# Performance work log

Measured on AMD Instinct MI355X. Metric: run time of the kernel, lower is better.

## Reference

```python
import math
import jax, jax.numpy as jnp
import numpy as np

B, N, NR, DA, E, H, NB = 2, 2048, 256, 256, 768, 12, 2
DH = E // H
NQ, NK = 32, 128
INF = 1e10


def _layernorm(x, g=None, b=None, eps=1e-5):
    mu = x.mean(-1, keepdims=True)
    var = ((x - mu) ** 2).mean(-1, keepdims=True)
    y = (x - mu) * jax.lax.rsqrt(var + eps)
    if g is not None:
        y = y * g + b
    return y


def _fourier(x):
    # NeRF-style: freqs = 2**linspace(0,12,64); out dim = 3*(1+2*64) = 387
    freqs = 2.0 ** jnp.linspace(0.0, 12.0, 64)
    ang = (x[..., None, :] * freqs[:, None]).reshape(*x.shape[:-1], -1)  # (...,192)
    return jnp.concatenate([x, jnp.sin(ang), jnp.cos(ang)], -1)


def _abs_pos(pos):
    # sinusoidal absolute PE, embed_dim=DA//2, include_input -> DA//2 + 1 dims
    d = DA // 2
    div = jnp.exp(jnp.arange(0, d, 2, dtype=jnp.float32) * (-math.log(10000.0) / d))
    ang = pos * div  # (B,N,1)*(d/2,) -> (B,N,d/2)
    return jnp.concatenate([pos, jnp.sin(ang), jnp.cos(ang)], -1)


def _local_bias(n, nq, nk):
    # vectorized create_local_attn_bias: block-diagonal local window mask
    i = jnp.arange(n)
    blk = i // nq
    lo = jnp.maximum(0, nq * blk - (nk - nq) // 2)
    hi = nq * blk + (nq + nk) // 2
    j = jnp.arange(n)
    allowed = (j[None, :] >= lo[:, None]) & (j[None, :] < hi[:, None])
    return jnp.where(allowed, 0.0, -INF).astype(jnp.float32)


def _rope(x, pos):
    # x: (B,H,N,DH), pos: (B,N) float
    half = DH // 2
    inv = 1.0 / (10000.0 ** (jnp.arange(half, dtype=jnp.float32) / half))
    ang = pos[:, None, :, None] * inv  # (B,1,N,half)
    c, s = jnp.cos(ang), jnp.sin(ang)
    x1, x2 = x[..., :half], x[..., half:]
    return jnp.concatenate([x1 * c - x2 * s, x1 * s + x2 * c], -1)


def setup_inputs() -> dict:
    key = jax.random.key(0)
    def rn(i, shape, s=1.0):
        return jax.random.normal(jax.random.fold_in(key, i), shape, jnp.float32) * s
    LF = 387 + (DA // 2 + 1) + 408  # 924
    tok = (jnp.arange(N) * NR) // N  # each atom's residue index (sorted)
    inp = {
        'atom_coords': rn(0, (B, N, 3), 10.0),
        'ref_pos': rn(1, (B, N, 3), 10.0),
        'res_id': jnp.broadcast_to(tok[None, :, None], (B, N, 1)).astype(jnp.int32),
        'res_type_feat': rn(2, (B, N, 23)),
        'charge': rn(3, (B, N, 1)),
        'atomic_number': rn(4, (B, N, 128)),
        'atom_name_feat': rn(5, (B, N, 256)),
        'adaLN_emb': rn(6, (B, DA)),
        'rope_pos': jnp.broadcast_to(jnp.arange(N, dtype=jnp.int32)[None], (B, N)),
        'atom_to_token': jnp.broadcast_to(jax.nn.one_hot(tok, NR, dtype=jnp.float32)[None], (B, N, NR)),
        'feat_W': rn(7, (LF, DA), 0.02), 'feat_b': jnp.zeros(DA), 'feat_ln_g': jnp.ones(DA), 'feat_ln_b': jnp.zeros(DA),
        'pos_W': rn(8, (387, DA), 0.02),
        'in_W': rn(9, (2 * DA, DA), 0.02),
        'tin_W': rn(10, (DA, E), 0.02), 'tin_b': jnp.zeros(E), 'tin_ln_g': jnp.ones(E), 'tin_ln_b': jnp.zeros(E),
        'ada_W': rn(11, (DA, E), 0.02), 'ada_b': jnp.zeros(E), 'ada_ln_g': jnp.ones(E), 'ada_ln_b': jnp.zeros(E),
        'blk_mod_W': rn(12, (NB, E, 6 * E), 0.02), 'blk_mod_b': jnp.zeros((NB, 6 * E)),
        'blk_qkv_W': rn(13, (NB, E, 3 * E), 0.02), 'blk_qkv_b': jnp.zeros((NB, 3 * E)),
        'blk_o_W': rn(14, (NB, E, E), 0.02), 'blk_o_b': jnp.zeros((NB, E)),
        'blk_m1_W': rn(15, (NB, E, 4 * E), 0.02), 'blk_m1_b': jnp.zeros((NB, 4 * E)),
        'blk_m2_W': rn(16, (NB, 4 * E, E), 0.02), 'blk_m2_b': jnp.zeros((NB, E)),
        'tout_W': rn(17, (E, DA), 0.02), 'tout_b': jnp.zeros(DA), 'tout_ln_g': jnp.ones(DA), 'tout_ln_b': jnp.zeros(DA),
    }
    return inp


def reference(atom_coords, ref_pos, res_id, res_type_feat, charge, atomic_number,
              atom_name_feat, adaLN_emb, rope_pos, atom_to_token,
              feat_W, feat_b, feat_ln_g, feat_ln_b, pos_W, in_W,
              tin_W, tin_b, tin_ln_g, tin_ln_b, ada_W, ada_b, ada_ln_g, ada_ln_b,
              blk_mod_W, blk_mod_b, blk_qkv_W, blk_qkv_b, blk_o_W, blk_o_b,
              blk_m1_W, blk_m1_b, blk_m2_W, blk_m2_b,
              tout_W, tout_b, tout_ln_g, tout_ln_b):
    # feature fusion
    ref_pos_emb = _fourier(ref_pos)                                   # (B,N,387)
    atom_res_pos = _abs_pos(res_id.astype(jnp.float32))               # (B,N,129)
    feats = jnp.concatenate([ref_pos_emb, res_type_feat, atom_res_pos,
                             charge, atomic_number, atom_name_feat], -1)  # (B,N,924)
    feats = jax.nn.silu(_layernorm(feats @ feat_W + feat_b, feat_ln_g, feat_ln_b))
    coords = _fourier(atom_coords) @ pos_W                            # (B,N,DA)
    atom_in = jnp.concatenate([feats, coords], -1) @ in_W             # (B,N,DA)
    x = _layernorm(atom_in @ tin_W + tin_b, tin_ln_g, tin_ln_b)       # (B,N,E)
    c = _layernorm(adaLN_emb @ ada_W + ada_b, ada_ln_g, ada_ln_b)     # (B,E)

    bias = _local_bias(N, NQ, NK)                                     # (N,N)
    pos = rope_pos.astype(jnp.float32)
    scale = 1.0 / math.sqrt(DH)
    for l in range(NB):  # small fixed layer count
        m = jax.nn.silu(c) @ blk_mod_W[l] + blk_mod_b[l]
        sh1, sc1, g1, sh2, sc2, g2 = jnp.split(m, 6, -1)              # each (B,E)
        h = _layernorm(x) * (1 + sc1[:, None]) + sh1[:, None]
        qkv = (h @ blk_qkv_W[l] + blk_qkv_b[l]).reshape(B, N, 3, H, DH)
        q, k, v = [qkv[:, :, i].transpose(0, 2, 1, 3) for i in range(3)]  # (B,H,N,DH)
        q, k = _rope(q, pos), _rope(k, pos)
        scores = jnp.einsum('bhqd,bhkd->bhqk', q, k) * scale + bias
        attn = jax.nn.softmax(scores, -1)
        o = jnp.einsum('bhqk,bhkd->bhqd', attn, v).transpose(0, 2, 1, 3).reshape(B, N, E)
        x = x + g1[:, None] * (o @ blk_o_W[l] + blk_o_b[l])
        h2 = _layernorm(x) * (1 + sc2[:, None]) + sh2[:, None]
        x = x + g2[:, None] * (jax.nn.gelu(h2 @ blk_m1_W[l] + blk_m1_b[l]) @ blk_m2_W[l] + blk_m2_b[l])

    atom_latent = _layernorm(x @ tout_W + tout_b, tout_ln_g, tout_ln_b)   # (B,N,DA)
    a2t = atom_to_token / (atom_to_token.sum(1, keepdims=True) + 1e-6)    # segment-mean weights
    residue_latent = jnp.einsum('bnr,bnd->brd', a2t, atom_latent)         # (B,NR,DA)
    return residue_latent, atom_latent
```

## Files before the change

### kernel.cpp

```cpp
#include <hip/hip_runtime.h>
#include <hip/hip_bf16.h>
#include <math.h>

#define B_ 2
#define N_ 2048
#define NR_ 256
#define DA_ 256
#define E_ 768
#define H_ 12
#define DH_ 64
#define NB_ 2

typedef __attribute__((ext_vector_type(8))) __bf16 bf16x8;
typedef __attribute__((ext_vector_type(4))) float f32x4;

union U8 { bf16x8 v; __hip_bfloat16 e[8]; unsigned short u[8]; };
union U4 { __hip_bfloat16 e[4]; uint2 u2; };

__device__ __forceinline__ void gload16(const void* g, void* l) {
    __builtin_amdgcn_global_load_lds(
        (const __attribute__((address_space(1))) void*)g,
        (__attribute__((address_space(3))) void*)l, 16, 0, 0);
}

__device__ __forceinline__ float bsum256(float v, float* red4, int tid) {
    #pragma unroll
    for (int m = 32; m > 0; m >>= 1) v += __shfl_xor(v, m, 64);
    __syncthreads();
    if ((tid & 63) == 0) red4[tid >> 6] = v;
    __syncthreads();
    return red4[0] + red4[1] + red4[2] + red4[3];
}

__global__ __launch_bounds__(128) void build_feats_kernel(
    const float* __restrict__ atom_coords, const float* __restrict__ ref_pos,
    const int* __restrict__ res_id, const float* __restrict__ res_type,
    const float* __restrict__ charge, const float* __restrict__ atomic_number,
    const float* __restrict__ atom_name, const int* __restrict__ rope_pos,
    __hip_bfloat16* __restrict__ feats, __hip_bfloat16* __restrict__ coordsF,
    float* __restrict__ ropeC, float* __restrict__ ropeS)
{
    int a = blockIdx.x;
    int tid = threadIdx.x;
    __hip_bfloat16* f  = feats   + (size_t)a * 1024;
    __hip_bfloat16* cf = coordsF + (size_t)a * 512;

    float rp[3], cc[3];
    #pragma unroll
    for (int i = 0; i < 3; ++i) { rp[i] = ref_pos[(size_t)a*3 + i]; cc[i] = atom_coords[(size_t)a*3 + i]; }

    if (tid < 3) { f[tid] = __float2bfloat16(rp[tid]); cf[tid] = __float2bfloat16(cc[tid]); }

    if (tid >= 64 && tid < 96) {
        int dd = tid - 64;
        float rpos = (float)rope_pos[a];
        float ang = rpos * expf(-0.28782313662425574f * (float)dd);
        float sn, cs; sincosf(ang, &sn, &cs);
        ropeC[a*32 + dd] = cs; ropeS[a*32 + dd] = sn;
    }

    for (int s = tid; s < 192; s += 128) {
        int fi = s / 3, ci = s % 3;
        float freq = exp2f(12.f * (float)fi / 63.f);
        float ar = rp[ci] * freq;
        float ac = cc[ci] * freq;
        float snr, csr, snc, csc_;
        sincosf(ar, &snr, &csr);
        sincosf(ac, &snc, &csc_);
        f[3 + s]    = __float2bfloat16(snr);  f[195 + s]  = __float2bfloat16(csr);
        cf[3 + s]   = __float2bfloat16(snc);  cf[195 + s] = __float2bfloat16(csc_);
    }
    if (tid < 23) f[387 + tid] = __float2bfloat16(res_type[(size_t)a*23 + tid]);

    float pos = (float)res_id[a];
    if (tid == 0) f[410] = __float2bfloat16(pos);
    if (tid < 64) {
        float div = expf(-9.210340371976184f / 128.f * (float)(2 * tid));
        float ang = pos * div;
        float sn, cs; sincosf(ang, &sn, &cs);
        f[411 + tid] = __float2bfloat16(sn);
        f[475 + tid] = __float2bfloat16(cs);
    }
    if (tid == 0) f[539] = __float2bfloat16(charge[a]);
    if (tid < 128) f[540 + tid] = __float2bfloat16(atomic_number[(size_t)a*128 + tid]);
    for (int s = tid; s < 256; s += 128) f[668 + s] = __float2bfloat16(atom_name[(size_t)a*256 + s]);
    if (tid < 100) f[924 + tid] = __float2bfloat16(0.f);
    if (tid < 125) cf[387 + tid] = __float2bfloat16(0.f);
}

__global__ __launch_bounds__(256) void transconv_kernel(
    const float* __restrict__ W, __hip_bfloat16* __restrict__ WT,
    int Ksrc, int Kdst, int Nn, size_t wstride, size_t tstride)
{
    __shared__ float t[32][33];
    W  += (size_t)blockIdx.z * wstride;
    WT += (size_t)blockIdx.z * tstride;
    int n0 = blockIdx.x * 32, k0 = blockIdx.y * 32;
    int tid = threadIdx.x;
    int tx = tid & 31, ty = tid >> 5;
    #pragma unroll
    for (int i = 0; i < 4; ++i) {
        int k = k0 + ty + i*8;
        t[ty + i*8][tx] = (k < Ksrc) ? W[(size_t)k * Nn + n0 + tx] : 0.f;
    }
    __syncthreads();
    #pragma unroll
    for (int i = 0; i < 4; ++i) {
        int row = ty + i*8;
        WT[(size_t)(n0 + row) * Kdst + k0 + tx] = __float2bfloat16(t[tx][row]);
    }
}

__device__ __forceinline__ float epi_apply(float v, int grow, int gcol,
    const float* bias, int mode, const float* X, int ldx,
    const float* gate, int gstride)
{
    if (bias) v += bias[gcol];
    if (mode == 1) {
        float u = 1.5957691216057308f * (v + 0.044715f * v * v * v);
        v = v / (1.f + __expf(-u));
    } else if (mode == 2) {
        int b = grow >> 11;
        v = X[(size_t)grow * ldx + gcol] + gate[(size_t)b * gstride + gcol] * v;
    } else if (mode == 3) {
        v = v * gate[grow];
    }
    return v;
}

__global__ __launch_bounds__(1024) void gemm_bf16_kernel(
    const __hip_bfloat16* __restrict__ A, int lda,
    const __hip_bfloat16* __restrict__ BT, int ldb,
    const float* __restrict__ bias,
    void* __restrict__ C, int ldc,
    int K, int mode, int obf,
    const float* __restrict__ X, int ldx,
    const float* __restrict__ gate, int gstride,
    float* __restrict__ P,
    int mtiles, size_t bstrideA, size_t bstrideB)
{
    __shared__ __hip_bfloat16 As[2][128 * 64];
    __shared__ __hip_bfloat16 Bs[2][128 * 64];

    int gx = gridDim.x;
    int nwg = gx * gridDim.y;
    int fo = blockIdx.y * gx + blockIdx.x;
    int ft = (fo & 7) * (nwg >> 3) + (fo >> 3);
    int bx = ft % gx, by = ft / gx;

    int bb  = by / mtiles;
    int m0l = (by % mtiles) * 128;
    int m0g = by * 128;
    int n0 = bx * 128;
    const __hip_bfloat16* Ab  = A  + (size_t)bb * bstrideA;
    const __hip_bfloat16* BTb = BT + (size_t)bb * bstrideB;
    int nz = gridDim.z;
    int Kh = K / nz;
    int kb = blockIdx.z * Kh;
    int tid = threadIdx.x;
    int w = tid >> 6, l = tid & 63;
    int wr = (w >> 2) * 32, wc = (w & 3) * 32;
    int lr = l & 15, lg = l >> 4;
    int skey = lr & 7;

    int rowS = tid >> 3;
    int gS   = (tid & 7) ^ (rowS & 7);

    f32x4 acc[2][2];
    #pragma unroll
    for (int i = 0; i < 2; ++i)
        #pragma unroll
        for (int j = 0; j < 2; ++j)
            acc[i][j] = f32x4{0.f, 0.f, 0.f, 0.f};

    gload16(Ab  + (size_t)(m0l + rowS) * lda + kb + gS * 8, (char*)As[0] + tid * 16);
    gload16(BTb + (size_t)(n0 + rowS) * ldb + kb + gS * 8, (char*)Bs[0] + tid * 16);

    int cur = 0;
    for (int k0 = kb; k0 < kb + Kh; k0 += 64) {
        __syncthreads();
        int kn = k0 + 64;
        if (kn < kb + Kh) {
            int nb = cur ^ 1;
            gload16(Ab  + (size_t)(m0l + rowS) * lda + kn + gS * 8, (char*)As[nb] + tid * 16);
            gload16(BTb + (size_t)(n0 + rowS) * ldb + kn + gS * 8, (char*)Bs[nb] + tid * 16);
        }
        #pragma unroll
        for (int ks = 0; ks < 2; ++ks) {
            int pch = ((ks*4 + lg) ^ skey) * 8;
            bf16x8 af[2], bfr[2];
            #pragma unroll
            for (int i = 0; i < 2; ++i)
                af[i]  = *(bf16x8*)(As[cur] + (wr + i*16 + lr) * 64 + pch);
            #pragma unroll
            for (int j = 0; j < 2; ++j)
                bfr[j] = *(bf16x8*)(Bs[cur] + (wc + j*16 + lr) * 64 + pch);
            #pragma unroll
            for (int i = 0; i < 2; ++i)
                #pragma unroll
                for (int j = 0; j < 2; ++j)
                    acc[i][j] = __builtin_amdgcn_mfma_f32_16x16x32_bf16(af[i], bfr[j], acc[i][j], 0, 0, 0);
        }
        cur ^= 1;
    }

    if (nz > 1) {
        int Nw = gridDim.x * 128;
        size_t pstride = (size_t)Nw * (gridDim.y * 128);
        float* Pz = P + (size_t)blockIdx.z * pstride;
        #pragma unroll
        for (int i = 0; i < 2; ++i)
            #pragma unroll
            for (int j = 0; j < 2; ++j)
                #pragma unroll
                for (int r = 0; r < 4; ++r) {
                    int grow = m0g + wr + i*16 + lg*4 + r;
                    int gcol = n0 + wc + j*16 + lr;
                    Pz[(size_t)grow * Nw + gcol] = acc[i][j][r];
                }
        return;
    }

    #pragma unroll
    for (int i = 0; i < 2; ++i)
        #pragma unroll
        for (int j = 0; j < 2; ++j)
            #pragma unroll
            for (int r = 0; r < 4; ++r) {
                int grow = m0g + wr + i*16 + lg*4 + r;
                int gcol = n0 + wc + j*16 + lr;
                float v = epi_apply(acc[i][j][r], grow, gcol, bias, mode, X, ldx, gate, gstride);
                if (obf)
                    ((__hip_bfloat16*)C)[(size_t)grow * ldc + gcol] = __float2bfloat16(v);
                else
                    ((float*)C)[(size_t)grow * ldc + gcol] = v;
            }
}

__global__ __launch_bounds__(256) void gcomb_kernel(
    const float* __restrict__ P, size_t pstride, int nz, int Nw,
    const float* __restrict__ bias,
    void* __restrict__ C, int ldc, int mode, int obf,
    const float* __restrict__ X, int ldx,
    const float* __restrict__ gate, int gstride,
    __hip_bfloat16* __restrict__ C2, int ldc2)
{
    int idx = blockIdx.x * 256 + threadIdx.x;
    int e0 = idx * 4;
    int grow = e0 / Nw, gc0 = e0 % Nw;
    float4 v = *(const float4*)(P + (size_t)grow * Nw + gc0);
    for (int z = 1; z < nz; ++z) {
        float4 t = *(const float4*)(P + (size_t)z * pstride + (size_t)grow * Nw + gc0);
        v.x += t.x; v.y += t.y; v.z += t.z; v.w += t.w;
    }
    float e[4] = {v.x, v.y, v.z, v.w};
    #pragma unroll
    for (int r = 0; r < 4; ++r)
        e[r] = epi_apply(e[r], grow, gc0 + r, bias, mode, X, ldx, gate, gstride);
    if (obf) {
        U4 o4;
        #pragma unroll
        for (int r = 0; r < 4; ++r) o4.e[r] = __float2bfloat16(e[r]);
        *(uint2*)((__hip_bfloat16*)C + (size_t)grow * ldc + gc0) = o4.u2;
    } else {
        *(float4*)((float*)C + (size_t)grow * ldc + gc0) = make_float4(e[0], e[1], e[2], e[3]);
    }
    if (C2) {
        U4 o4;
        #pragma unroll
        for (int r = 0; r < 4; ++r) o4.e[r] = __float2bfloat16(e[r]);
        *(uint2*)(C2 + (size_t)grow * ldc2 + gc0) = o4.u2;
    }
}

__global__ __launch_bounds__(256) void combln256_kernel(
    const float* __restrict__ P, size_t pstride, int nz,
    const float* __restrict__ bias,
    const float* __restrict__ g, const float* __restrict__ bv,
    int do_silu, int obf,
    void* __restrict__ out, int ldout)
{
    int row = blockIdx.x, d = threadIdx.x;
    __shared__ float red4[4];
    float v = P[(size_t)row*256 + d];
    for (int z = 1; z < nz; ++z) v += P[(size_t)z*pstride + (size_t)row*256 + d];
    v += bias[d];
    float mu = bsum256(v, red4, d) * (1.f/256.f);
    float dv = v - mu;
    float rstd = rsqrtf(bsum256(dv*dv, red4, d) * (1.f/256.f) + 1e-5f);
    float y = dv * rstd * g[d] + bv[d];
    if (do_silu) y = y / (1.f + __expf(-y));
    if (obf) ((__hip_bfloat16*)out)[(size_t)row * ldout + d] = __float2bfloat16(y);
    else     ((float*)out)[(size_t)row * ldout + d] = y;
}

__global__ __launch_bounds__(256) void tinfuse_kernel(
    const float* __restrict__ P, size_t pstride, int nz,
    const float* __restrict__ bias,
    const float* __restrict__ g, const float* __restrict__ bb,
    const float* __restrict__ scm, const float* __restrict__ shm,
    float* __restrict__ X, __hip_bfloat16* __restrict__ Hb)
{
    int row = blockIdx.x, tid = threadIdx.x;
    int b = row >> 11;
    __shared__ float red4[4];
    float tv[3];
    float s = 0.f;
    #pragma unroll
    for (int q = 0; q < 3; ++q) {
        int d = tid + q*256;
        float v = P[(size_t)row*768 + d];
        for (int z = 1; z < nz; ++z) v += P[(size_t)z*pstride + (size_t)row*768 + d];
        v += bias[d];
        tv[q] = v; s += v;
    }
    float mu1 = bsum256(s, red4, tid) * (1.f/768.f);
    float s2 = 0.f;
    #pragma unroll
    for (int q = 0; q < 3; ++q) { float dv = tv[q] - mu1; s2 += dv*dv; }
    float rstd1 = rsqrtf(bsum256(s2, red4, tid) * (1.f/768.f) + 1e-5f);
    float xv[3];
    float s3 = 0.f;
    #pragma unroll
    for (int q = 0; q < 3; ++q) {
        int d = tid + q*256;
        float y = (tv[q] - mu1) * rstd1 * g[d] + bb[d];
        X[(size_t)row*768 + d] = y;
        xv[q] = y; s3 += y;
    }
    float mu2 = bsum256(s3, red4, tid) * (1.f/768.f);
    float s4 = 0.f;
    #pragma unroll
    for (int q = 0; q < 3; ++q) { float dv = xv[q] - mu2; s4 += dv*dv; }
    float rstd2 = rsqrtf(bsum256(s4, red4, tid) * (1.f/768.f) + 1e-5f);
    #pragma unroll
    for (int q = 0; q < 3; ++q) {
        int d = tid + q*256;
        float h = (xv[q] - mu2) * rstd2 * (1.f + scm[(size_t)b*4608 + d]) + shm[(size_t)b*4608 + d];
        Hb[(size_t)row*768 + d] = __float2bfloat16(h);
    }
}

__global__ __launch_bounds__(256) void gcombln_kernel(
    const float* __restrict__ P, size_t pstride, int nz,
    const float* __restrict__ bias,
    float* __restrict__ X,
    const float* __restrict__ gate,
    const float* __restrict__ scm, const float* __restrict__ shm,
    __hip_bfloat16* __restrict__ Hb)
{
    int row = blockIdx.x, tid = threadIdx.x;
    int b = row >> 11;
    __shared__ float red4[4];
    float xv[3];
    float s = 0.f;
    #pragma unroll
    for (int q = 0; q < 3; ++q) {
        int d = tid + q*256;
        float v = P[(size_t)row*768 + d];
        for (int z = 1; z < nz; ++z) v += P[(size_t)z*pstride + (size_t)row*768 + d];
        v += bias[d];
        v = X[(size_t)row*768 + d] + gate[(size_t)b*4608 + d] * v;
        X[(size_t)row*768 + d] = v;
        xv[q] = v; s += v;
    }
    float mu = bsum256(s, red4, tid) * (1.f/768.f);
    float s2 = 0.f;
    #pragma unroll
    for (int q = 0; q < 3; ++q) { float dv = xv[q] - mu; s2 += dv*dv; }
    float rstd = rsqrtf(bsum256(s2, red4, tid) * (1.f/768.f) + 1e-5f);
    #pragma unroll
    for (int q = 0; q < 3; ++q) {
        int d = tid + q*256;
        float y = (xv[q] - mu) * rstd * (1.f + scm[(size_t)b*4608 + d]) + shm[(size_t)b*4608 + d];
        Hb[(size_t)row*768 + d] = __float2bfloat16(y);
    }
}

__global__ __launch_bounds__(256) void ada_kernel(
    const float* __restrict__ emb, const float* __restrict__ W,
    const float* __restrict__ bias,
    const float* __restrict__ g, const float* __restrict__ bb,
    float* __restrict__ c, float* __restrict__ c_silu)
{
    int b = blockIdx.x, tid = threadIdx.x;
    __shared__ float emb_s[256];
    __shared__ float t[768];
    __shared__ float red[256];
    emb_s[tid] = emb[b*256 + tid];
    __syncthreads();
    for (int q = 0; q < 3; ++q) {
        int e = tid + q*256;
        float acc = bias[e];
        for (int k = 0; k < 256; ++k) acc += emb_s[k] * W[(size_t)k*768 + e];
        t[e] = acc;
    }
    __syncthreads();
    float s = 0.f; for (int q = 0; q < 3; ++q) s += t[tid + q*256];
    red[tid] = s; __syncthreads();
    for (int off = 128; off > 0; off >>= 1) { if (tid < off) red[tid] += red[tid+off]; __syncthreads(); }
    float mu = red[0] / 768.f; __syncthreads();
    float s2 = 0.f; for (int q = 0; q < 3; ++q) { float d = t[tid + q*256] - mu; s2 += d*d; }
    red[tid] = s2; __syncthreads();
    for (int off = 128; off > 0; off >>= 1) { if (tid < off) red[tid] += red[tid+off]; __syncthreads(); }
    float rstd = rsqrtf(red[0] / 768.f + 1e-5f);
    for (int q = 0; q < 3; ++q) {
        int e = tid + q*256;
        float y = (t[e] - mu) * rstd * g[e] + bb[e];
        c[b*768 + e] = y;
        c_silu[b*768 + e] = y / (1.f + expf(-y));
    }
}

__global__ __launch_bounds__(256) void mod2_kernel(
    const float* __restrict__ c_silu, const float* __restrict__ mod_W,
    float* __restrict__ part)
{
    int idx = blockIdx.x * 256 + threadIdx.x;
    int z = blockIdx.y;
    int lyr = idx / 9216, b = (idx / 4608) & 1, j = idx % 4608;
    const float* Wl = mod_W + (size_t)lyr * 768 * 4608;
    const float* cs = c_silu + b * 768;
    float acc = 0.f;
    int k0 = z * 192;
    for (int k = k0; k < k0 + 192; ++k) acc += cs[k] * Wl[(size_t)k * 4608 + j];
    part[(size_t)z * 18432 + idx] = acc;
}

__global__ __launch_bounds__(256) void modc_kernel(
    const float* __restrict__ part, const float* __restrict__ mod_b,
    float* __restrict__ m2buf)
{
    int idx = blockIdx.x * 256 + threadIdx.x;
    int lyr = idx / 9216, j = idx % 4608;
    float acc = mod_b[(size_t)lyr * 4608 + j];
    #pragma unroll
    for (int z = 0; z < 4; ++z) acc += part[(size_t)z * 18432 + idx];
    m2buf[idx] = acc;
}

__global__ __launch_bounds__(256) void attn_mfma_kernel(
    const __hip_bfloat16* __restrict__ qkv,
    const float* __restrict__ ropeC,
    const float* __restrict__ ropeS,
    __hip_bfloat16* __restrict__ o)
{
    int bid = blockIdx.x;
    int qg = bid & 15;
    int h  = (bid >> 4) % 12;
    int b  = bid / 192;
    int tid = threadIdx.x;
    int w  = tid >> 6;
    int l  = tid & 63;
    int lr = l & 15, lg = l >> 4;

    int qb = qg * 4 + w;
    int lo_blk = max(0, 128*qg - 48);
    int hi_blk = min(N_, 128*qg + 176);
    int lo = max(0, 32*qb - 48);
    int hi = min(N_, 32*qb + 80);
    int wlen = hi - lo;
    int offv = lo - lo_blk;

    __shared__ __hip_bfloat16 Vl[224 * 72];
    __shared__ __hip_bfloat16 Pl[4 * 32 * 144];
    __hip_bfloat16* Plw = Pl + w * (32 * 144);

    {
        int vr0 = tid >> 3;
        int c0  = (tid & 7) * 8;
        #pragma unroll
        for (int it = 0; it < 7; ++it) {
            int vr = it*32 + vr0;
            int n = lo_blk + vr;
            U8 v;
            if (n < hi_blk) {
                v.v = *(const bf16x8*)(qkv + ((size_t)(b*N_ + n))*2304 + 1536 + h*64 + c0);
            } else {
                #pragma unroll
                for (int j = 0; j < 8; ++j) v.u[j] = 0;
            }
            *(bf16x8*)(Vl + vr*72 + c0) = v.v;
        }
    }

    bf16x8 aq0[2], aq1[2];
    #pragma unroll
    for (int i = 0; i < 2; ++i) {
        int n = qb*32 + i*16 + lr;
        const __hip_bfloat16* qrow = qkv + ((size_t)(b*N_ + n))*2304 + h*64;
        U8 xlo, xhi;
        xlo.v = *(const bf16x8*)(qrow + lg*8);
        xhi.v = *(const bf16x8*)(qrow + 32 + lg*8);
        const float* pc = ropeC + ((size_t)(b*N_ + n))*32 + lg*8;
        const float* ps = ropeS + ((size_t)(b*N_ + n))*32 + lg*8;
        float4 c0 = *(const float4*)(pc), c1 = *(const float4*)(pc + 4);
        float4 s0 = *(const float4*)(ps), s1 = *(const float4*)(ps + 4);
        float cv[8] = {c0.x,c0.y,c0.z,c0.w,c1.x,c1.y,c1.z,c1.w};
        float sv[8] = {s0.x,s0.y,s0.z,s0.w,s1.x,s1.y,s1.z,s1.w};
        U8 f0, f1;
        #pragma unroll
        for (int j = 0; j < 8; ++j) {
            float x1 = __bfloat162float(xlo.e[j]);
            float x2 = __bfloat162float(xhi.e[j]);
            f0.e[j] = __float2bfloat16(x1*cv[j] - x2*sv[j]);
            f1.e[j] = __float2bfloat16(x1*sv[j] + x2*cv[j]);
        }
        aq0[i] = f0.v; aq1[i] = f1.v;
    }

    f32x4 S[2][8];
    #pragma unroll
    for (int i = 0; i < 2; ++i)
        #pragma unroll
        for (int jt = 0; jt < 8; ++jt)
            S[i][jt] = f32x4{0.f, 0.f, 0.f, 0.f};

    #pragma unroll
    for (int jt = 0; jt < 8; ++jt) {
        int n = lo + jt*16 + lr;
        U8 f0, f1;
        if (n < hi) {
            const __hip_bfloat16* krow = qkv + ((size_t)(b*N_ + n))*2304 + 768 + h*64;
            U8 xlo, xhi;
            xlo.v = *(const bf16x8*)(krow + lg*8);
            xhi.v = *(const bf16x8*)(krow + 32 + lg*8);
            const float* pc = ropeC + ((size_t)(b*N_ + n))*32 + lg*8;
            const float* ps = ropeS + ((size_t)(b*N_ + n))*32 + lg*8;
            float4 c0 = *(const float4*)(pc), c1 = *(const float4*)(pc + 4);
            float4 s0 = *(const float4*)(ps), s1 = *(const float4*)(ps + 4);
            float cv[8] = {c0.x,c0.y,c0.z,c0.w,c1.x,c1.y,c1.z,c1.w};
            float sv[8] = {s0.x,s0.y,s0.z,s0.w,s1.x,s1.y,s1.z,s1.w};
            #pragma unroll
            for (int j = 0; j < 8; ++j) {
                float x1 = __bfloat162float(xlo.e[j]);
                float x2 = __bfloat162float(xhi.e[j]);
                f0.e[j] = __float2bfloat16(x1*cv[j] - x2*sv[j]);
                f1.e[j] = __float2bfloat16(x1*sv[j] + x2*cv[j]);
            }
        } else {
            #pragma unroll
            for (int j = 0; j < 8; ++j) { f0.u[j] = 0; f1.u[j] = 0; }
        }
        #pragma unroll
        for (int i = 0; i < 2; ++i) {
            S[i][jt] = __builtin_amdgcn_mfma_f32_16x16x32_bf16(aq0[i], f0.v, S[i][jt], 0, 0, 0);
            S[i][jt] = __builtin_amdgcn_mfma_f32_16x16x32_bf16(aq1[i], f1.v, S[i][jt], 0, 0, 0);
        }
    }

    #pragma unroll
    for (int jt = 0; jt < 8; ++jt) {
        bool oob = (jt*16 + lr) >= wlen;
        #pragma unroll
        for (int i = 0; i < 2; ++i)
            #pragma unroll
            for (int r = 0; r < 4; ++r)
                S[i][jt][r] = oob ? -1e30f : S[i][jt][r] * 0.125f;
    }

    float rinv[2][4];
    #pragma unroll
    for (int i = 0; i < 2; ++i) {
        #pragma unroll
        for (int r = 0; r < 4; ++r) {
            float m = -1e30f;
            #pragma unroll
            for (int jt = 0; jt < 8; ++jt) m = fmaxf(m, S[i][jt][r]);
            #pragma unroll
            for (int mask = 8; mask > 0; mask >>= 1) m = fmaxf(m, __shfl_xor(m, mask, 16));
            float sum = 0.f;
            #pragma unroll
            for (int jt = 0; jt < 8; ++jt) {
                float e = __expf(S[i][jt][r] - m);
                S[i][jt][r] = e;
                sum += e;
            }
            #pragma unroll
            for (int mask = 8; mask > 0; mask >>= 1) sum += __shfl_xor(sum, mask, 16);
            rinv[i][r] = 1.f / sum;
        }
    }

    #pragma unroll
    for (int i = 0; i < 2; ++i)
        #pragma unroll
        for (int jt = 0; jt < 8; ++jt)
            #pragma unroll
            for (int r = 0; r < 4; ++r) {
                int row = i*16 + lg*4 + r;
                int colp = (jt*16 + lr) ^ (lg << 3);
                Plw[row*144 + colp] = __float2bfloat16(S[i][jt][r]);
            }

    __syncthreads();

    f32x4 O_[2][4];
    #pragma unroll
    for (int i = 0; i < 2; ++i)
        #pragma unroll
        for (int ct = 0; ct < 4; ++ct)
            O_[i][ct] = f32x4{0.f, 0.f, 0.f, 0.f};

    int key = (lr >> 2) & 3;
    #pragma unroll
    for (int kt = 0; kt < 4; ++kt) {
        bf16x8 pa[2];
        #pragma unroll
        for (int i = 0; i < 2; ++i) {
            int row = i*16 + lr;
            int colp = (kt*32 + lg*8) ^ (key << 3);
            pa[i] = *(bf16x8*)(Plw + row*144 + colp);
        }
        #pragma unroll
        for (int ct = 0; ct < 4; ++ct) {
            U8 bv;
            #pragma unroll
            for (int j = 0; j < 8; ++j)
                bv.e[j] = Vl[(offv + kt*32 + lg*8 + j)*72 + ct*16 + lr];
            O_[0][ct] = __builtin_amdgcn_mfma_f32_16x16x32_bf16(pa[0], bv.v, O_[0][ct], 0, 0, 0);
            O_[1][ct] = __builtin_amdgcn_mfma_f32_16x16x32_bf16(pa[1], bv.v, O_[1][ct], 0, 0, 0);
        }
    }

    #pragma unroll
    for (int i = 0; i < 2; ++i)
        #pragma unroll
        for (int ct = 0; ct < 4; ++ct)
            #pragma unroll
            for (int r = 0; r < 4; ++r) {
                int row = qb*32 + i*16 + lg*4 + r;
                o[((size_t)(b*N_ + row))*768 + h*64 + ct*16 + lr] =
                    __float2bfloat16(O_[i][ct][r] * rinv[i][r]);
            }
}

__global__ __launch_bounds__(256) void a2t_transpose_kernel(
    const float* __restrict__ a2t, __hip_bfloat16* __restrict__ a2tTb)
{
    __shared__ float t[32][33];
    int r0 = blockIdx.x * 32, n0 = blockIdx.y * 32, b = blockIdx.z;
    int tid = threadIdx.x;
    int tx = tid & 31, ty = tid >> 5;
    #pragma unroll
    for (int i = 0; i < 4; ++i) {
        int row = ty + i*8;
        t[row][tx] = a2t[((size_t)b*N_ + n0 + row) * 256 + r0 + tx];
    }
    __syncthreads();
    #pragma unroll
    for (int i = 0; i < 4; ++i) {
        int row = ty + i*8;
        a2tTb[((size_t)b*256 + r0 + row) * N_ + n0 + tx] = __float2bfloat16(t[tx][row]);
    }
}

__global__ __launch_bounds__(256) void rowrecip_kernel(
    const __hip_bfloat16* __restrict__ a2tTb, float* __restrict__ recip)
{
    int row = blockIdx.x;
    int tid = threadIdx.x;
    __shared__ float red4[4];
    U8 v; v.v = *(const bf16x8*)(a2tTb + (size_t)row*2048 + tid*8);
    float s = 0.f;
    #pragma unroll
    for (int j = 0; j < 8; ++j) s += __bfloat162float(v.e[j]);
    float tot = bsum256(s, red4, tid);
    if (tid == 0) recip[row] = 1.f / (tot + 1e-6f);
}

extern "C" void kernel_launch(void* const* d_in, const int* in_sizes, int n_in,
                              void* d_out, int out_size, void* d_ws, size_t ws_size,
                              hipStream_t stream) {
    const float* atom_coords  = (const float*)d_in[0];
    const float* ref_pos      = (const float*)d_in[1];
    const int*   res_id       = (const int*)  d_in[2];
    const float* res_type     = (const float*)d_in[3];
    const float* charge       = (const float*)d_in[4];
    const float* atomic_num   = (const float*)d_in[5];
    const float* atom_name    = (const float*)d_in[6];
    const float* adaLN_emb    = (const float*)d_in[7];
    const int*   rope_pos     = (const int*)  d_in[8];
    const float* atom_to_tok  = (const float*)d_in[9];
    const float* feat_W       = (const float*)d_in[10];
    const float* feat_b       = (const float*)d_in[11];
    const float* feat_ln_g    = (const float*)d_in[12];
    const float* feat_ln_b    = (const float*)d_in[13];
    const float* pos_W        = (const float*)d_in[14];
    const float* in_W         = (const float*)d_in[15];
    const float* tin_W        = (const float*)d_in[16];
    const float* tin_b        = (const float*)d_in[17];
    const float* tin_ln_g     = (const float*)d_in[18];
    const float* tin_ln_b     = (const float*)d_in[19];
    const float* ada_W        = (const float*)d_in[20];
    const float* ada_b        = (const float*)d_in[21];
    const float* ada_ln_g     = (const float*)d_in[22];
    const float* ada_ln_b     = (const float*)d_in[23];
    const float* blk_mod_W    = (const float*)d_in[24];
    const float* blk_mod_b    = (const float*)d_in[25];
    const float* blk_qkv_W    = (const float*)d_in[26];
    const float* blk_qkv_b    = (const float*)d_in[27];
    const float* blk_o_W      = (const float*)d_in[28];
    const float* blk_o_b      = (const float*)d_in[29];
    const float* blk_m1_W     = (const float*)d_in[30];
    const float* blk_m1_b     = (const float*)d_in[31];
    const float* blk_m2_W     = (const float*)d_in[32];
    const float* blk_m2_b     = (const float*)d_in[33];
    const float* tout_W       = (const float*)d_in[34];
    const float* tout_b       = (const float*)d_in[35];
    const float* tout_ln_g    = (const float*)d_in[36];
    const float* tout_ln_b    = (const float*)d_in[37];

    const int BN = B_ * N_;
    float* ws = (float*)d_ws;

    const size_t OFF_X    = 0;
    const size_t OFF_HB   = OFF_X    + (size_t)BN*768;
    const size_t OFF_QKVB = OFF_HB   + (size_t)BN*768/2;
    const size_t OFF_OB   = OFF_QKVB + (size_t)BN*2304/2;
    const size_t OFF_UB   = OFF_OB   + (size_t)BN*768/2;
    const size_t OFF_WTL  = OFF_UB   + (size_t)BN*3072/2;
    const size_t WTL_FLTS = (size_t)(2*768*2304 + 2*768*768 + 2*768*3072 + 2*3072*768) / 2;
    const size_t OFF_WTS  = OFF_WTL  + WTL_FLTS;
    const size_t OFF_RC   = OFF_WTS  + 524288;
    const size_t OFF_RS   = OFF_RC   + (size_t)BN*32;
    const size_t OFF_SM   = OFF_RS   + (size_t)BN*32;

    float* X = ws + OFF_X;
    __hip_bfloat16* Hb   = (__hip_bfloat16*)(ws + OFF_HB);
    __hip_bfloat16* QKVb = (__hip_bfloat16*)(ws + OFF_QKVB);
    __hip_bfloat16* Ob   = (__hip_bfloat16*)(ws + OFF_OB);
    __hip_bfloat16* Ub   = (__hip_bfloat16*)(ws + OFF_UB);
    __hip_bfloat16* WTL  = (__hip_bfloat16*)(ws + OFF_WTL);
    __hip_bfloat16* WTs  = (__hip_bfloat16*)(ws + OFF_WTS);
    float* ropeC  = ws + OFF_RC;
    float* ropeS  = ws + OFF_RS;
    float* cbuf   = ws + OFF_SM;
    float* c_silu = cbuf + 1536;
    float* mbuf2  = c_silu + 1536;
    float* modpart= mbuf2 + 18432;

    __hip_bfloat16* WTqkv = WTL;
    __hip_bfloat16* WTo   = WTqkv + (size_t)2*768*2304;
    __hip_bfloat16* WTm1  = WTo   + (size_t)2*768*768;
    __hip_bfloat16* WTm2  = WTm1  + (size_t)2*768*3072;

    __hip_bfloat16* WTfeat = WTs;
    __hip_bfloat16* WTpos  = WTfeat + (size_t)1024*256;
    __hip_bfloat16* WTin   = WTpos  + (size_t)512*256;
    __hip_bfloat16* WTtin  = WTin   + (size_t)512*256;
    __hip_bfloat16* WTtout = WTtin  + (size_t)256*768;

    __hip_bfloat16* featsB  = QKVb;
    __hip_bfloat16* coordsB = QKVb + (size_t)BN*1024;
    float* t1               = ws + OFF_UB;
    __hip_bfloat16* concatB = (__hip_bfloat16*)(t1 + (size_t)BN*256);
    __hip_bfloat16* atom_inB= Ob;

    __hip_bfloat16* a2tTb   = Ob;
    __hip_bfloat16* latTb   = Ob + (size_t)2*256*2048;
    float* recip            = modpart;

    float* P_pa   = ws + OFF_X;
    float* P_tin  = ws + OFF_UB;
    float* P_o    = ws + OFF_UB;
    float* P_m2   = ws + OFF_QKVB;
    float* P_tout = ws + OFF_UB;
    float* P_res  = ws + OFF_UB;

    float* out_res = (float*)d_out;
    float* out_lat = out_res + (size_t)B_*NR_*DA_;

    ada_kernel<<<2, 256, 0, stream>>>(adaLN_emb, ada_W, ada_b, ada_ln_g, ada_ln_b,
        cbuf, c_silu);
    mod2_kernel<<<dim3(72, 4), 256, 0, stream>>>(c_silu, blk_mod_W, modpart);
    modc_kernel<<<72, 256, 0, stream>>>(modpart, blk_mod_b, mbuf2);

    transconv_kernel<<<dim3(72, 24, 2), 256, 0, stream>>>(blk_qkv_W, WTqkv,
        768, 768, 2304, (size_t)768*2304, (size_t)768*2304);
    transconv_kernel<<<dim3(24, 24, 2), 256, 0, stream>>>(blk_o_W, WTo,
        768, 768, 768, (size_t)768*768, (size_t)768*768);
    transconv_kernel<<<dim3(96, 24, 2), 256, 0, stream>>>(blk_m1_W, WTm1,
        768, 768, 3072, (size_t)768*3072, (size_t)768*3072);
    transconv_kernel<<<dim3(24, 96, 2), 256, 0, stream>>>(blk_m2_W, WTm2,
        3072, 3072, 768, (size_t)3072*768, (size_t)3072*768);
    transconv_kernel<<<dim3(8, 32), 256, 0, stream>>>(feat_W, WTfeat, 924, 1024, 256, 0, 0);
    transconv_kernel<<<dim3(8, 16), 256, 0, stream>>>(pos_W,  WTpos,  387, 512, 256, 0, 0);
    transconv_kernel<<<dim3(8, 16), 256, 0, stream>>>(in_W,   WTin,   512, 512, 256, 0, 0);
    transconv_kernel<<<dim3(24, 8), 256, 0, stream>>>(tin_W,  WTtin,  256, 256, 768, 0, 0);
    transconv_kernel<<<dim3(8, 24), 256, 0, stream>>>(tout_W, WTtout, 768, 768, 256, 0, 0);

    build_feats_kernel<<<BN, 128, 0, stream>>>(atom_coords, ref_pos, res_id,
        res_type, charge, atomic_num, atom_name, rope_pos, featsB, coordsB,
        ropeC, ropeS);

    gemm_bf16_kernel<<<dim3(2, 32, 4), 1024, 0, stream>>>(featsB, 1024, WTfeat, 1024, nullptr,
        nullptr, 0, 1024, 0, 0, nullptr, 0, nullptr, 0, P_pa, 32, 0, 0);
    combln256_kernel<<<BN, 256, 0, stream>>>(P_pa, (size_t)BN*256, 4, feat_b,
        feat_ln_g, feat_ln_b, 1, 1, concatB, 512);
    gemm_bf16_kernel<<<dim3(2, 32, 4), 1024, 0, stream>>>(coordsB, 512, WTpos, 512, nullptr,
        nullptr, 0, 512, 0, 0, nullptr, 0, nullptr, 0, P_pa, 32, 0, 0);
    gcomb_kernel<<<1024, 256, 0, stream>>>(P_pa, (size_t)BN*256, 4, 256, nullptr,
        concatB + 256, 512, 0, 1, nullptr, 0, nullptr, 0, nullptr, 0);
    gemm_bf16_kernel<<<dim3(2, 32, 4), 1024, 0, stream>>>(concatB, 512, WTin, 512, nullptr,
        nullptr, 0, 512, 0, 0, nullptr, 0, nullptr, 0, P_pa, 32, 0, 0);
    gcomb_kernel<<<1024, 256, 0, stream>>>(P_pa, (size_t)BN*256, 4, 256, nullptr,
        atom_inB, 256, 0, 1, nullptr, 0, nullptr, 0, nullptr, 0);
    gemm_bf16_kernel<<<dim3(6, 32, 2), 1024, 0, stream>>>(atom_inB, 256, WTtin, 256, nullptr,
        nullptr, 0, 256, 0, 0, nullptr, 0, nullptr, 0, P_tin, 32, 0, 0);
    tinfuse_kernel<<<BN, 256, 0, stream>>>(P_tin, (size_t)BN*768, 2, tin_b,
        tin_ln_g, tin_ln_b, mbuf2 + 768, mbuf2 + 0, X, Hb);

    for (int l = 0; l < NB_; ++l) {
        const float* qkvB = blk_qkv_b + (size_t)l*2304;
        const float* oB   = blk_o_b   + (size_t)l*768;
        const float* m1B  = blk_m1_b  + (size_t)l*3072;
        const float* m2B  = blk_m2_b  + (size_t)l*768;
        __hip_bfloat16* Wq = WTqkv + (size_t)l*768*2304;
        __hip_bfloat16* Wo = WTo   + (size_t)l*768*768;
        __hip_bfloat16* W1 = WTm1  + (size_t)l*768*3072;
        __hip_bfloat16* W2 = WTm2  + (size_t)l*3072*768;

        float* mptr = mbuf2 + (size_t)l*9216;
        float* sh2 = mptr + 2304, *sc2 = mptr + 3072;
        float* g1  = mptr + 1536, *g2 = mptr + 3840;

        gemm_bf16_kernel<<<dim3(18, 32, 1), 1024, 0, stream>>>(Hb, 768, Wq, 768, qkvB,
            QKVb, 2304, 768, 0, 1, nullptr, 0, nullptr, 0, nullptr, 32, 0, 0);
        attn_mfma_kernel<<<B_*H_*16, 256, 0, stream>>>(QKVb, ropeC, ropeS, Ob);
        gemm_bf16_kernel<<<dim3(6, 32, 2), 1024, 0, stream>>>(Ob, 768, Wo, 768, nullptr,
            nullptr, 0, 768, 0, 0, nullptr, 0, nullptr, 0, P_o, 32, 0, 0);
        gcombln_kernel<<<BN, 256, 0, stream>>>(P_o, (size_t)BN*768, 2, oB,
            X, g1, sc2, sh2, Hb);
        gemm_bf16_kernel<<<dim3(24, 32, 1), 1024, 0, stream>>>(Hb, 768, W1, 768, m1B,
            Ub, 3072, 768, 1, 1, nullptr, 0, nullptr, 0, nullptr, 32, 0, 0);
        gemm_bf16_kernel<<<dim3(6, 32, 2), 1024, 0, stream>>>(Ub, 3072, W2, 3072, nullptr,
            nullptr, 0, 3072, 0, 0, nullptr, 0, nullptr, 0, P_m2, 32, 0, 0);
        if (l < NB_ - 1) {
            float* mnext = mbuf2 + (size_t)(l+1)*9216;
            gcombln_kernel<<<BN, 256, 0, stream>>>(P_m2, (size_t)BN*768, 2, m2B,
                X, g2, mnext + 768, mnext + 0, Hb);
        } else {
            gcomb_kernel<<<3072, 256, 0, stream>>>(P_m2, (size_t)BN*768, 2, 768, m2B,
                Hb, 768, 2, 1, X, 768, g2, 4608, nullptr, 0);
        }
    }

    gemm_bf16_kernel<<<dim3(2, 32, 4), 1024, 0, stream>>>(Hb, 768, WTtout, 768, nullptr,
        nullptr, 0, 768, 0, 0, nullptr, 0, nullptr, 0, P_tout, 32, 0, 0);
    combln256_kernel<<<BN, 256, 0, stream>>>(P_tout, (size_t)BN*256, 4, tout_b,
        tout_ln_g, tout_ln_b, 0, 0, out_lat, 256);

    a2t_transpose_kernel<<<dim3(8, 64, 2), 256, 0, stream>>>(atom_to_tok, a2tTb);
    rowrecip_kernel<<<512, 256, 0, stream>>>(a2tTb, recip);
    transconv_kernel<<<dim3(8, 64, 2), 256, 0, stream>>>(out_lat, latTb, 2048, 2048, 256,
        (size_t)2048*256, (size_t)256*2048);
    gemm_bf16_kernel<<<dim3(2, 4, 8), 1024, 0, stream>>>(a2tTb, 2048, latTb, 2048, nullptr,
        nullptr, 0, 2048, 0, 0, nullptr, 0, nullptr, 0, P_res,
        2, (size_t)256*2048, (size_t)256*2048);
    gcomb_kernel<<<128, 256, 0, stream>>>(P_res, (size_t)512*256, 8, 256, nullptr,
        out_res, 256, 3, 0, nullptr, 0, recip, 0, nullptr, 0);
}
```

Baseline: 497.0 us.

## Deepen GEMM pipeline to 4-stage K=32 ring with explicit vmcnt waits

The bf16 GEMM kernel moves from a double-buffered K=64 tile to a four-slot ring of K=32 tiles, keeping three tiles in flight. Each wait uses an explicit s_waitcnt vmcnt plus a raw s_barrier. Half the threads now load A and half load B, with a new XOR swizzle for the 32-wide rows. The aim is to hide global-to-LDS latency better, at the cost of twice as many barriers per K and less MFMA work between syncs. Kh is assumed to be a multiple of 32 and at least 96.

Result: no change. 494.7 us (median of 2 runs) (-0.5%).

```diff
diff --git a/kernel.cpp b/kernel.cpp
--- a/kernel.cpp
+++ b/kernel.cpp
@@ -139,8 +139,8 @@
     float* __restrict__ P,
     int mtiles, size_t bstrideA, size_t bstrideB)
 {
-    __shared__ __hip_bfloat16 As[2][128 * 64];
-    __shared__ __hip_bfloat16 Bs[2][128 * 64];
+    __shared__ __hip_bfloat16 As[4][128 * 32];
+    __shared__ __hip_bfloat16 Bs[4][128 * 32];
 
     int gx = gridDim.x;
     int nwg = gx * gridDim.y;
@@ -161,10 +161,14 @@
     int w = tid >> 6, l = tid & 63;
     int wr = (w >> 2) * 32, wc = (w & 3) * 32;
     int lr = l & 15, lg = l >> 4;
-    int skey = lr & 7;
-
-    int rowS = tid >> 3;
-    int gS   = (tid & 7) ^ (rowS & 7);
+    int slot = ((lg ^ ((lr >> 1) & 3)) & 3) * 8;
+
+    int sop  = tid >> 9;
+    int seg  = tid & 511;
+    int rowS = seg >> 2;
+    int gS   = (seg & 3) ^ ((rowS >> 1) & 3);
+    const __hip_bfloat16* srcBase = sop ? (BTb + (size_t)(n0 + rowS) * ldb)
+                                        : (Ab  + (size_t)(m0l + rowS) * lda);
 
     f32x4 acc[2][2];
     #pragma unroll
@@ -173,35 +177,38 @@
         for (int j = 0; j < 2; ++j)
             acc[i][j] = f32x4{0.f, 0.f, 0.f, 0.f};
 
-    gload16(Ab  + (size_t)(m0l + rowS) * lda + kb + gS * 8, (char*)As[0] + tid * 16);
-    gload16(BTb + (size_t)(n0 + rowS) * ldb + kb + gS * 8, (char*)Bs[0] + tid * 16);
-
-    int cur = 0;
-    for (int k0 = kb; k0 < kb + Kh; k0 += 64) {
-        __syncthreads();
-        int kn = k0 + 64;
-        if (kn < kb + Kh) {
-            int nb = cur ^ 1;
-            gload16(Ab  + (size_t)(m0l + rowS) * lda + kn + gS * 8, (char*)As[nb] + tid * 16);
-            gload16(BTb + (size_t)(n0 + rowS) * ldb + kn + gS * 8, (char*)Bs[nb] + tid * 16);
+    int nt = Kh >> 5;
+
+    #pragma unroll
+    for (int t = 0; t < 3; ++t)
+        gload16(srcBase + kb + t*32 + gS * 8,
+                (char*)(sop ? Bs[t] : As[t]) + seg * 16);
+
+    for (int i = 0; i < nt; ++i) {
+        int rem = nt - 1 - i;
+        if (rem >= 2)      asm volatile("s_waitcnt vmcnt(2)" ::: "memory");
+        else if (rem == 1) asm volatile("s_waitcnt vmcnt(1)" ::: "memory");
+        else               asm volatile("s_waitcnt vmcnt(0)" ::: "memory");
+        __builtin_amdgcn_s_barrier();
+        asm volatile("" ::: "memory");
+        if (i + 3 < nt) {
+            int nb = (i + 3) & 3;
+            gload16(srcBase + kb + (i+3)*32 + gS * 8,
+                    (char*)(sop ? Bs[nb] : As[nb]) + seg * 16);
         }
-        #pragma unroll
-        for (int ks = 0; ks < 2; ++ks) {
-            int pch = ((ks*4 + lg) ^ skey) * 8;
-            bf16x8 af[2], bfr[2];
-            #pragma unroll
-            for (int i = 0; i < 2; ++i)
-                af[i]  = *(bf16x8*)(As[cur] + (wr + i*16 + lr) * 64 + pch);
+        int cb = i & 3;
+        bf16x8 af[2], bfr[2];
+        #pragma unroll
+        for (int i2 = 0; i2 < 2; ++i2)
+            af[i2]  = *(bf16x8*)(As[cb] + (wr + i2*16 + lr) * 32 + slot);
+        #pragma unroll
+        for (int j = 0; j < 2; ++j)
+            bfr[j] = *(bf16x8*)(Bs[cb] + (wc + j*16 + lr) * 32 + slot);
+        #pragma unroll
+        for (int i2 = 0; i2 < 2; ++i2)
             #pragma unroll
             for (int j = 0; j < 2; ++j)
-                bfr[j] = *(bf16x8*)(Bs[cur] + (wc + j*16 + lr) * 64 + pch);
-            #pragma unroll
-            for (int i = 0; i < 2; ++i)
-                #pragma unroll
-                for (int j = 0; j < 2; ++j)
-                    acc[i][j] = __builtin_amdgcn_mfma_f32_16x16x32_bf16(af[i], bfr[j], acc[i][j], 0, 0, 0);
-        }
-        cur ^= 1;
+                acc[i2][j] = __builtin_amdgcn_mfma_f32_16x16x32_bf16(af[i2], bfr[j], acc[i2][j], 0, 0, 0);
     }
 
     if (nz > 1) {
```

## Split GEMM k-slices across wave halves with 32x64 warp tiles and LDS reduction

Applied to the files above, without the earlier changes.

The 16 waves of the 128x128 GEMM block are now split into two groups of eight. Each group handles one 32-wide k-half of every 64-wide K step, and each wave owns a 32x64 output tile instead of 32x32. At the end the second group writes its partial accumulators to LDS, the first group adds them and runs the epilogue alone. This is meant to cut repeated A-fragment LDS reads per MFMA and improve reuse. In exchange it adds an extra barrier, an LDS reduction pass, and an epilogue run by only half the waves, and the launch-bounds hint is raised.

New measurement: 531.3 us. +6.9%, slower.

```diff
diff --git a/kernel.cpp b/kernel.cpp
--- a/kernel.cpp
+++ b/kernel.cpp
@@ -128,7 +128,7 @@
     return v;
 }
 
-__global__ __launch_bounds__(1024) void gemm_bf16_kernel(
+__global__ __launch_bounds__(1024, 8) void gemm_bf16_kernel(
     const __hip_bfloat16* __restrict__ A, int lda,
     const __hip_bfloat16* __restrict__ BT, int ldb,
     const float* __restrict__ bias,
@@ -139,8 +139,7 @@
     float* __restrict__ P,
     int mtiles, size_t bstrideA, size_t bstrideB)
 {
-    __shared__ __hip_bfloat16 As[2][128 * 64];
-    __shared__ __hip_bfloat16 Bs[2][128 * 64];
+    __shared__ __hip_bfloat16 Sm[4][128 * 64];
 
     int gx = gridDim.x;
     int nwg = gx * gridDim.y;
@@ -159,22 +158,25 @@
     int kb = blockIdx.z * Kh;
     int tid = threadIdx.x;
     int w = tid >> 6, l = tid & 63;
-    int wr = (w >> 2) * 32, wc = (w & 3) * 32;
+    int pos = w & 7;
+    int kh  = w >> 3;
+    int wr = (pos >> 1) * 32, wc = (pos & 1) * 64;
     int lr = l & 15, lg = l >> 4;
     int skey = lr & 7;
+    int pch = ((kh*4 + lg) ^ skey) * 8;
 
     int rowS = tid >> 3;
     int gS   = (tid & 7) ^ (rowS & 7);
 
-    f32x4 acc[2][2];
+    f32x4 acc[2][4];
     #pragma unroll
     for (int i = 0; i < 2; ++i)
         #pragma unroll
-        for (int j = 0; j < 2; ++j)
+        for (int j = 0; j < 4; ++j)
             acc[i][j] = f32x4{0.f, 0.f, 0.f, 0.f};
 
-    gload16(Ab  + (size_t)(m0l + rowS) * lda + kb + gS * 8, (char*)As[0] + tid * 16);
-    gload16(BTb + (size_t)(n0 + rowS) * ldb + kb + gS * 8, (char*)Bs[0] + tid * 16);
+    gload16(Ab  + (size_t)(m0l + rowS) * lda + kb + gS * 8, (char*)Sm[0] + tid * 16);
+    gload16(BTb + (size_t)(n0 + rowS) * ldb + kb + gS * 8, (char*)Sm[2] + tid * 16);
 
     int cur = 0;
     for (int k0 = kb; k0 < kb + Kh; k0 += 64) {
@@ -182,27 +184,37 @@
         int kn = k0 + 64;
         if (kn < kb + Kh) {
             int nb = cur ^ 1;
-            gload16(Ab  + (size_t)(m0l + rowS) * lda + kn + gS * 8, (char*)As[nb] + tid * 16);
-            gload16(BTb + (size_t)(n0 + rowS) * ldb + kn + gS * 8, (char*)Bs[nb] + tid * 16);
-        }
-        #pragma unroll
-        for (int ks = 0; ks < 2; ++ks) {
-            int pch = ((ks*4 + lg) ^ skey) * 8;
-            bf16x8 af[2], bfr[2];
-            #pragma unroll
-            for (int i = 0; i < 2; ++i)
-                af[i]  = *(bf16x8*)(As[cur] + (wr + i*16 + lr) * 64 + pch);
-            #pragma unroll
-            for (int j = 0; j < 2; ++j)
-                bfr[j] = *(bf16x8*)(Bs[cur] + (wc + j*16 + lr) * 64 + pch);
-            #pragma unroll
-            for (int i = 0; i < 2; ++i)
-                #pragma unroll
-                for (int j = 0; j < 2; ++j)
-                    acc[i][j] = __builtin_amdgcn_mfma_f32_16x16x32_bf16(af[i], bfr[j], acc[i][j], 0, 0, 0);
+            gload16(Ab  + (size_t)(m0l + rowS) * lda + kn + gS * 8, (char*)Sm[nb] + tid * 16);
+            gload16(BTb + (size_t)(n0 + rowS) * ldb + kn + gS * 8, (char*)Sm[2+nb] + tid * 16);
+        }
+        bf16x8 af[2];
+        af[0] = *(bf16x8*)(Sm[cur] + (wr + lr) * 64 + pch);
+        af[1] = *(bf16x8*)(Sm[cur] + (wr + 16 + lr) * 64 + pch);
+        #pragma unroll
+        for (int j = 0; j < 4; ++j) {
+            bf16x8 bfr = *(bf16x8*)(Sm[2+cur] + (wc + j*16 + lr) * 64 + pch);
+            acc[0][j] = __builtin_amdgcn_mfma_f32_16x16x32_bf16(af[0], bfr, acc[0][j], 0, 0, 0);
+            acc[1][j] = __builtin_amdgcn_mfma_f32_16x16x32_bf16(af[1], bfr, acc[1][j], 0, 0, 0);
         }
         cur ^= 1;
     }
+
+    __syncthreads();
+    f32x4* red = (f32x4*)Sm;
+    if (kh) {
+        #pragma unroll
+        for (int i = 0; i < 2; ++i)
+            #pragma unroll
+            for (int j = 0; j < 4; ++j)
+                red[(pos*8 + i*4 + j)*64 + l] = acc[i][j];
+    }
+    __syncthreads();
+    if (kh) return;
+    #pragma unroll
+    for (int i = 0; i < 2; ++i)
+        #pragma unroll
+        for (int j = 0; j < 4; ++j)
+            acc[i][j] += red[(pos*8 + i*4 + j)*64 + l];
 
     if (nz > 1) {
         int Nw = gridDim.x * 128;
@@ -211,7 +223,7 @@
         #pragma unroll
         for (int i = 0; i < 2; ++i)
             #pragma unroll
-            for (int j = 0; j < 2; ++j)
+            for (int j = 0; j < 4; ++j)
                 #pragma unroll
                 for (int r = 0; r < 4; ++r) {
                     int grow = m0g + wr + i*16 + lg*4 + r;
@@ -224,7 +236,7 @@
     #pragma unroll
     for (int i = 0; i < 2; ++i)
         #pragma unroll
-        for (int j = 0; j < 2; ++j)
+        for (int j = 0; j < 4; ++j)
             #pragma unroll
             for (int r = 0; r < 4; ++r) {
                 int grow = m0g + wr + i*16 + lg*4 + r;
```
